# Kernel optimization log

Measured on AMD Instinct MI355X. Metric: run time of the kernel, lower is better.

## Reference

```python
import jax, jax.numpy as jnp
import numpy as np

N = 100000      # nodes
E = 3200000     # edges (avg degree 32)
NFEAT = 512
NHID = 256
NCLASS = 40
NLAYERS = 8
T1 = 5
T2 = 5
G1 = 1
G2 = 1
BETA = 0.5      # weight_beta
LAMDA = 0.5
ALPHA = 0.1
EPS = 1e-5


def ortho_trans(weight, T, groups):
    """Newton-Schulz orthogonalization (Ortho_Trans.forward)."""
    g = groups
    Z = weight.reshape(g, weight.shape[0] // g, -1)          # [g, d, k]
    Zc = Z - Z.mean(axis=-1, keepdims=True)
    S = jnp.einsum('gik,gjk->gij', Zc, Zc)                   # covariance [g, d, d]
    eye = jnp.eye(S.shape[-1], dtype=S.dtype)
    S = S + EPS * eye
    norm_S = jnp.sqrt(jnp.sum(S * S, axis=(1, 2), keepdims=True))  # fro norm
    S = S / norm_S
    B0 = jnp.broadcast_to(eye, S.shape)

    def body(B, _):
        B3 = B @ B @ B                                       # matrix_power3
        return 1.5 * B - 0.5 * (B3 @ S), None                # baddbmm(1.5,B,-0.5,B3,S)

    Bt, _ = jax.lax.scan(body, B0, None, length=T)
    W = (Bt @ Zc) / jnp.sqrt(norm_S)
    return W.reshape(weight.shape)


def setup_inputs() -> dict:
    key = jax.random.key(0)
    ks = jax.random.split(key, 8)
    stdv = 1.0 / np.sqrt(NHID)
    return {
        'x': jax.random.normal(ks[0], (N, NFEAT), dtype=jnp.float32),
        'edge_src': jax.random.randint(ks[1], (E,), 0, N, dtype=jnp.int32),
        'edge_dst': jax.random.randint(ks[2], (E,), 0, N, dtype=jnp.int32),
        'edge_weight': jax.random.uniform(ks[3], (E,), dtype=jnp.float32),
        'W0': jax.random.normal(ks[4], (NHID, NFEAT), dtype=jnp.float32) * 0.05,
        'b0': jnp.zeros((NHID,), dtype=jnp.float32),
        'convW': jax.random.uniform(ks[5], (NLAYERS, NHID, NHID), dtype=jnp.float32,
                                    minval=-stdv, maxval=stdv),
        'W1': jax.random.normal(ks[6], (NCLASS, NHID), dtype=jnp.float32) * 0.05,
        'b1': jnp.zeros((NCLASS,), dtype=jnp.float32),
    }


def reference(x, edge_src, edge_dst, edge_weight, W0, b0, convW, W1, b1):
    # fcs[0].weight is orthogonalized at init (Ortho=True)
    W0o = ortho_trans(W0, T1, G1)
    h = jax.nn.relu(x @ W0o.T + b0)                          # [N, NHID]
    h0 = h
    I = jnp.eye(NHID, dtype=h.dtype)
    ls = jnp.arange(1, NLAYERS + 1, dtype=h.dtype)

    def layer(h, inp):
        W, l = inp
        theta = jnp.log(LAMDA / l + 1.0)
        # sparse spmm: hi = adj @ h
        msgs = edge_weight[:, None] * h[edge_src]            # [E, NHID]
        hi = jax.ops.segment_sum(msgs, edge_dst, num_segments=N)
        support = (1.0 - ALPHA) * hi + ALPHA * h0            # variant=False -> r == support
        we = BETA * W + (1.0 - BETA) * I
        t = ortho_trans(we, T2, G2)
        out = jax.nn.relu(theta * (support @ t) + (1.0 - theta) * support)
        return out, None

    h, _ = jax.lax.scan(layer, h, (convW, ls))
    logits = h @ W1.T + b1
    return jax.nn.log_softmax(logits, axis=1)
```

## Files before the change

kernel.cpp:

```cpp
#include <hip/hip_runtime.h>
#include <math.h>

#define NNODES 100000
#define NEDGE  3200000
#define NF     512
#define NH     256
#define NC     40
#define NLAY   8
#define EPSV   1e-5f

#define NBUK 782
#define EPB  16384
#define BCAP 6144

typedef __attribute__((ext_vector_type(8))) short short8;
typedef __attribute__((ext_vector_type(4))) float floatx4;



__device__ __forceinline__ float block_sum_256(float v) {
    __shared__ float sb[8];
    #pragma unroll
    for (int off = 32; off; off >>= 1) v += __shfl_down(v, off, 64);
    if ((threadIdx.x & 63) == 0) sb[threadIdx.x >> 6] = v;
    __syncthreads();
    return sb[0] + sb[1] + sb[2] + sb[3];
}

__device__ __forceinline__ unsigned short bf16_rte(float a) {
    unsigned int u = __float_as_uint(a);
    return (unsigned short)((u + 0x7fffu + ((u >> 16) & 1u)) >> 16);
}
__device__ __forceinline__ unsigned int pack_bf2(float a, float b) {
    unsigned int ua = __float_as_uint(a), ub = __float_as_uint(b);
    ua = (ua + 0x7fffu + ((ua >> 16) & 1u)) >> 16;
    ub = (ub + 0x7fffu + ((ub >> 16) & 1u)) & 0xffff0000u;
    return ua | ub;
}


__global__ void k_hist(const int* __restrict__ dst, int* __restrict__ counts, int n) {
    int i = blockIdx.x * 256 + threadIdx.x;
    if (i < n) atomicAdd(&counts[dst[i]], 1);
}

__global__ void k_scan1(const int* __restrict__ in, int* __restrict__ out,
                        int* __restrict__ bsum, int n) {
    __shared__ int s[1024];
    int t = threadIdx.x, g = blockIdx.x * 1024 + t;
    int v = (g < n) ? in[g] : 0;
    s[t] = v; __syncthreads();
    for (int off = 1; off < 1024; off <<= 1) {
        int u = (t >= off) ? s[t - off] : 0;
        __syncthreads();
        s[t] += u;
        __syncthreads();
    }
    if (g < n) out[g] = s[t] - v;
    if (t == 1023) bsum[blockIdx.x] = s[1023];
}

__global__ void k_scan2(int* __restrict__ bsum, int nb) {
    __shared__ int s[128];
    int t = threadIdx.x;
    int v = (t < nb) ? bsum[t] : 0;
    s[t] = v; __syncthreads();
    for (int off = 1; off < 128; off <<= 1) {
        int u = (t >= off) ? s[t - off] : 0;
        __syncthreads();
        s[t] += u;
        __syncthreads();
    }
    if (t < nb) bsum[t] = s[t] - v;
}

__global__ void k_scan3(int* __restrict__ out, const int* __restrict__ bsum, int n) {
    int g = blockIdx.x * 1024 + threadIdx.x;
    if (g < n) out[g] += bsum[blockIdx.x];
}

__global__ void k_initcur(const int* __restrict__ rstart, int* __restrict__ gcur) {
    int b = blockIdx.x * 256 + threadIdx.x;
    if (b < NBUK) gcur[b] = rstart[b << 7];
}

__global__ __launch_bounds__(1024) void k_binA(const int* __restrict__ src,
                                               const int* __restrict__ dst,
                                               const float* __restrict__ w,
                                               int* __restrict__ gcur,
                                               uint2* __restrict__ gstage) {
    __shared__ int lhist[1024];
    __shared__ int lrun[NBUK];
    __shared__ int lcnt[NBUK];
    const int t = threadIdx.x;
    lhist[t] = 0;
    if (t < NBUK) lcnt[t] = 0;
    __syncthreads();
    const int e0 = blockIdx.x * EPB;
    unsigned int pk[16]; int bk[16]; int dl[16];
    #pragma unroll
    for (int i = 0; i < 16; i++) {
        int e = e0 + i * 1024 + t;
        bk[i] = -1;
        if (e < NEDGE) {
            int d = dst[e];
            bk[i] = d >> 7; dl[i] = d & 127;
            unsigned int wb = bf16_rte(w[e]) & 0x7FFFu;
            pk[i] = ((unsigned int)src[e] << 15) | wb;
            atomicAdd(&lhist[bk[i]], 1);
        }
    }
    __syncthreads();
    if (t < NBUK) {
        int c = lhist[t];
        if (c > 0) lrun[t] = atomicAdd(&gcur[t], c);
    }
    __syncthreads();
    #pragma unroll
    for (int i = 0; i < 16; i++) {
        if (bk[i] >= 0) {
            int p = lrun[bk[i]] + atomicAdd(&lcnt[bk[i]], 1);
            gstage[p] = make_uint2(pk[i], (unsigned int)dl[i]);
        }
    }
}

__global__ __launch_bounds__(256) void k_binB(const int* __restrict__ rstart,
                                              const uint2* __restrict__ gstage,
                                              unsigned int* __restrict__ epack) {
    __shared__ unsigned int  spk[BCAP];
    __shared__ unsigned char sdl[BCAP];
    __shared__ unsigned int  lout[BCAP];
    __shared__ int lh[256];
    const int b = blockIdx.x, t = threadIdx.x;
    const int base = rstart[b << 7];
    const int nn = (b + 1) << 7;
    const int end = (nn < NNODES) ? rstart[nn] : NEDGE;
    const int cnt = end - base;
    lh[t] = 0;
    __syncthreads();
    for (int i = t; i < cnt; i += 256) {
        uint2 e = gstage[base + i];
        spk[i] = e.x;
        int d = (int)(e.y & 127u);
        sdl[i] = (unsigned char)d;
        atomicAdd(&lh[d], 1);
    }
    __syncthreads();
    int v = lh[t];
    for (int off = 1; off < 256; off <<= 1) {
        int u = (t >= off) ? lh[t - off] : 0;
        __syncthreads();
        lh[t] += u;
        __syncthreads();
    }
    int excl = lh[t] - v;
    __syncthreads();
    lh[t] = excl;
    __syncthreads();
    for (int i = t; i < cnt; i += 256) {
        int p = atomicAdd(&lh[sdl[i]], 1);
        lout[p] = spk[i];
    }
    __syncthreads();
    for (int i = t; i < cnt; i += 256) epack[base + i] = lout[i];
}


__global__ void k_xbf16(const float* __restrict__ X, unsigned short* __restrict__ Xb, long n8) {
    long i = (long)blockIdx.x * 256 + threadIdx.x;
    if (i >= n8) return;
    const float* p = X + i * 8;
    float4 a = *(const float4*)p;
    float4 b = *(const float4*)(p + 4);
    uint4 o;
    o.x = pack_bf2(a.x, a.y); o.y = pack_bf2(a.z, a.w);
    o.z = pack_bf2(b.x, b.y); o.w = pack_bf2(b.z, b.w);
    *(uint4*)(Xb + i * 8) = o;
}


__global__ void k_zc0(const float* __restrict__ W0, float* __restrict__ Zc0) {
    int r = blockIdx.x, t = threadIdx.x;
    float a = W0[r * NF + t];
    float b = W0[r * NF + 256 + t];
    float mean = block_sum_256(a + b) * (1.0f / 512.0f);
    Zc0[r * NF + t]       = a - mean;
    Zc0[r * NF + 256 + t] = b - mean;
}

__global__ void k_zcC(const float* __restrict__ convW, float* __restrict__ ZcC) {
    int g = blockIdx.x >> 8, r = blockIdx.x & 255, t = threadIdx.x;
    float v = 0.5f * convW[((size_t)g * NH + r) * NH + t] + ((r == t) ? 0.5f : 0.0f);
    float mean = block_sum_256(v) * (1.0f / 256.0f);
    ZcC[((size_t)g * NH + r) * NH + t] = v - mean;
}

__global__ __launch_bounds__(256) void k_gram(const float* __restrict__ Zc0,
                                              const float* __restrict__ ZcC,
                                              float* __restrict__ S) {
    const int b = blockIdx.z;
    const float* A = (b == 0) ? Zc0 : (ZcC + (size_t)(b - 1) * 65536);
    const int K = (b == 0) ? 512 : 256;
    const int r0 = blockIdx.y * 64, c0 = blockIdx.x * 64;
    __shared__ float As[32][76], Bs[32][76];
    const int t = threadIdx.x, tx = t & 15, ty = t >> 4;
    const int lr = t >> 2, lk = (t & 3) * 4;
    float acc[4][4] = {};
    for (int k0 = 0; k0 < K; k0 += 32) {
        float4 a0 = *(const float4*)(A + (size_t)(r0 + lr) * K + k0 + lk);
        float4 a1 = *(const float4*)(A + (size_t)(r0 + lr) * K + k0 + lk + 16);
        As[lk + 0][lr] = a0.x; As[lk + 1][lr] = a0.y; As[lk + 2][lr] = a0.z; As[lk + 3][lr] = a0.w;
        As[lk + 16][lr] = a1.x; As[lk + 17][lr] = a1.y; As[lk + 18][lr] = a1.z; As[lk + 19][lr] = a1.w;
        float4 b0 = *(const float4*)(A + (size_t)(c0 + lr) * K + k0 + lk);
        float4 b1 = *(const float4*)(A + (size_t)(c0 + lr) * K + k0 + lk + 16);
        Bs[lk + 0][lr] = b0.x; Bs[lk + 1][lr] = b0.y; Bs[lk + 2][lr] = b0.z; Bs[lk + 3][lr] = b0.w;
        Bs[lk + 16][lr] = b1.x; Bs[lk + 17][lr] = b1.y; Bs[lk + 18][lr] = b1.z; Bs[lk + 19][lr] = b1.w;
        __syncthreads();
        #pragma unroll
        for (int kk = 0; kk < 32; kk++) {
            float a[4], bb[4];
            *(float4*)&a[0]  = *(const float4*)&As[kk][ty * 4];
            *(float4*)&bb[0] = *(const float4*)&Bs[kk][tx * 4];
            #pragma unroll
            for (int i = 0; i < 4; i++)
                #pragma unroll
                for (int j = 0; j < 4; j++) acc[i][j] = fmaf(a[i], bb[j], acc[i][j]);
        }
        __syncthreads();
    }
    #pragma unroll
    for (int i = 0; i < 4; i++)
        #pragma unroll
        for (int j = 0; j < 4; j++) {
            int r = r0 + ty * 4 + i, c = c0 + tx * 4 + j;
            float v = acc[i][j];
            if (r == c) v += EPSV;
            S[(size_t)b * 65536 + r * NH + c] = v;
        }
}

__global__ void k_fro(const float* __restrict__ S, float* __restrict__ scales) {
    __shared__ float sb[8];
    const int b = blockIdx.x, t = threadIdx.x;
    const float* p = S + (size_t)b * 65536;
    float s = 0.f;
    for (int i = t; i < 65536; i += 256) { float v = p[i]; s = fmaf(v, v, s); }
    #pragma unroll
    for (int off = 32; off; off >>= 1) s += __shfl_down(s, off, 64);
    if ((t & 63) == 0) sb[t >> 6] = s;
    __syncthreads();
    if (t == 0) {
        float nrm = sqrtf(sb[0] + sb[1] + sb[2] + sb[3]);
        scales[b]      = 1.0f / nrm;
        scales[16 + b] = rsqrtf(nrm);
    }
}

__global__ void k_initB1(const float* __restrict__ S, const float* __restrict__ scales,
                         float* __restrict__ B) {
    int i = blockIdx.x * 256 + threadIdx.x;
    int b = i >> 16, m = i & 65535;
    float v = -0.5f * scales[b] * S[i];
    if ((m >> 8) == (m & 255)) v += 1.5f;
    B[i] = v;
}

__global__ __launch_bounds__(256) void k_ns_pair(const float* __restrict__ Bb,
                                                 const float* __restrict__ Smat,
                                                 float* __restrict__ T1b,
                                                 float* __restrict__ T2b) {
    const int b = blockIdx.z;
    const int bb = (b < 9) ? b : b - 9;
    const float* A  = Bb + (size_t)bb * 65536;
    const float* Bm = (b < 9) ? A : (Smat + (size_t)bb * 65536);
    float* C = (b < 9) ? (T1b + (size_t)bb * 65536) : (T2b + (size_t)bb * 65536);
    const int r0 = blockIdx.y * 64, c0 = blockIdx.x * 64;
    __shared__ float As[32][76], Bs[32][76];
    const int t = threadIdx.x, tx = t & 15, ty = t >> 4;
    const int lr = t >> 2, lk = (t & 3) * 4;
    const int bk = t >> 3, bc = (t & 7) * 8;
    float acc[4][4] = {};
    for (int k0 = 0; k0 < 256; k0 += 32) {
        float4 a0 = *(const float4*)(A + (size_t)(r0 + lr) * 256 + k0 + lk);
        float4 a1 = *(const float4*)(A + (size_t)(r0 + lr) * 256 + k0 + lk + 16);
        As[lk + 0][lr] = a0.x; As[lk + 1][lr] = a0.y; As[lk + 2][lr] = a0.z; As[lk + 3][lr] = a0.w;
        As[lk + 16][lr] = a1.x; As[lk + 17][lr] = a1.y; As[lk + 18][lr] = a1.z; As[lk + 19][lr] = a1.w;
        float4 b0 = *(const float4*)(Bm + (size_t)(k0 + bk) * 256 + c0 + bc);
        float4 b1 = *(const float4*)(Bm + (size_t)(k0 + bk) * 256 + c0 + bc + 4);
        *(float4*)&Bs[bk][bc]     = b0;
        *(float4*)&Bs[bk][bc + 4] = b1;
        __syncthreads();
        #pragma unroll
        for (int kk = 0; kk < 32; kk++) {
            float a[4], bb2[4];
            *(float4*)&a[0]   = *(const float4*)&As[kk][ty * 4];
            *(float4*)&bb2[0] = *(const float4*)&Bs[kk][tx * 4];
            #pragma unroll
            for (int i = 0; i < 4; i++)
                #pragma unroll
                for (int j = 0; j < 4; j++) acc[i][j] = fmaf(a[i], bb2[j], acc[i][j]);
        }
        __syncthreads();
    }
    #pragma unroll
    for (int i = 0; i < 4; i++)
        #pragma unroll
        for (int j = 0; j < 4; j++)
            C[(size_t)(r0 + ty * 4 + i) * 256 + c0 + tx * 4 + j] = acc[i][j];
}

__global__ __launch_bounds__(256) void k_small_nn(const float* __restrict__ A0,
                                                  const float* __restrict__ B0,
                                                  float* __restrict__ C0,
                                                  int sA, int sB, int sC,
                                                  int K, int Ncols, int mode,
                                                  const float* __restrict__ scale) {
    const int b = blockIdx.z;
    const float* A = A0 + (size_t)b * sA;
    const float* Bm = B0 + (size_t)b * sB;
    float* C = C0 + (size_t)b * sC;
    const int r0 = blockIdx.y * 64, c0 = blockIdx.x * 64;
    __shared__ float As[32][76], Bs[32][76];
    const int t = threadIdx.x, tx = t & 15, ty = t >> 4;
    const int lr = t >> 2, lk = (t & 3) * 4;
    const int bk = t >> 3, bc = (t & 7) * 8;
    float acc[4][4] = {};
    for (int k0 = 0; k0 < K; k0 += 32) {
        float4 a0 = *(const float4*)(A + (size_t)(r0 + lr) * K + k0 + lk);
        float4 a1 = *(const float4*)(A + (size_t)(r0 + lr) * K + k0 + lk + 16);
        As[lk + 0][lr] = a0.x; As[lk + 1][lr] = a0.y; As[lk + 2][lr] = a0.z; As[lk + 3][lr] = a0.w;
        As[lk + 16][lr] = a1.x; As[lk + 17][lr] = a1.y; As[lk + 18][lr] = a1.z; As[lk + 19][lr] = a1.w;
        float4 b0 = *(const float4*)(Bm + (size_t)(k0 + bk) * Ncols + c0 + bc);
        float4 b1 = *(const float4*)(Bm + (size_t)(k0 + bk) * Ncols + c0 + bc + 4);
        *(float4*)&Bs[bk][bc]     = b0;
        *(float4*)&Bs[bk][bc + 4] = b1;
        __syncthreads();
        #pragma unroll
        for (int kk = 0; kk < 32; kk++) {
            float a[4], bb[4];
            *(float4*)&a[0]  = *(const float4*)&As[kk][ty * 4];
            *(float4*)&bb[0] = *(const float4*)&Bs[kk][tx * 4];
            #pragma unroll
            for (int i = 0; i < 4; i++)
                #pragma unroll
                for (int j = 0; j < 4; j++) acc[i][j] = fmaf(a[i], bb[j], acc[i][j]);
        }
        __syncthreads();
    }
    #pragma unroll
    for (int i = 0; i < 4; i++)
        #pragma unroll
        for (int j = 0; j < 4; j++) {
            size_t idx = (size_t)(r0 + ty * 4 + i) * Ncols + c0 + tx * 4 + j;
            if (mode == 1) C[idx] = 1.5f * C[idx] - 0.5f * scale[b] * acc[i][j];
            else C[idx] = scale[b] * acc[i][j];
        }
}


__global__ void k_prepM(const float* __restrict__ tbuf, unsigned short* __restrict__ Mpack) {
    int idx = blockIdx.x * 256 + threadIdx.x;
    int lane = idx & 63;
    int tg   = (idx >> 6) & 15;
    int s    = (idx >> 10) & 1;
    int c    = (idx >> 11) & 3;
    int l    = idx >> 13;
    float theta = logf(0.5f / (float)(l + 1) + 1.0f);
    float mtheta = 1.0f - theta;
    int n  = tg * 16 + (lane & 15);
    int k0 = c * 64 + s * 32 + (lane >> 4) * 8;
    const float* T = tbuf + (size_t)l * 65536;
    unsigned short o[8];
    #pragma unroll
    for (int j = 0; j < 8; j++) {
        int kp = k0 + j;
        int kn = (kp & 0xC0) | ((kp & 3) << 4) | ((kp >> 2) & 15);
        float v = theta * T[(size_t)kn * 256 + n] + ((kn == n) ? mtheta : 0.0f);
        o[j] = bf16_rte(v);
    }
    *(uint4*)(Mpack + (size_t)idx * 8) = *(uint4*)o;
}

__global__ void k_prepW0(const float* __restrict__ W0o, unsigned short* __restrict__ Wpack) {
    int idx = blockIdx.x * 256 + threadIdx.x;
    int lane = idx & 63;
    int tg   = (idx >> 6) & 15;
    int s    = (idx >> 10) & 1;
    int c    = idx >> 11;
    int n  = tg * 16 + (lane & 15);
    int k0 = c * 64 + s * 32 + (lane >> 4) * 8;
    const float* p = W0o + (size_t)n * NF + k0;
    unsigned short o[8];
    #pragma unroll
    for (int j = 0; j < 8; j++) o[j] = bf16_rte(p[j]);
    *(uint4*)(Wpack + (size_t)idx * 8) = *(uint4*)o;
}


__global__ __launch_bounds__(256) void k_fc0_mfma(const unsigned short* __restrict__ Xb,
                                                  const unsigned short* __restrict__ Wp,
                                                  const float* __restrict__ bias,
                                                  unsigned char* __restrict__ h0u8,
                                                  float* __restrict__ h0scale) {
    __shared__ int rmax[64];
    const int t = threadIdx.x, lane = t & 63, w = t >> 6;
    const int q = lane >> 4, m = lane & 15;
    const int r0 = blockIdx.x * 64;
    if (t < 64) rmax[t] = 0;
    floatx4 acc[4][4] = {};
    #pragma unroll
    for (int c = 0; c < 8; c++) {
        #pragma unroll
        for (int s = 0; s < 2; s++) {
            short8 afr[4];
            #pragma unroll
            for (int i = 0; i < 4; i++) {
                int row = r0 + i * 16 + m; if (row > NNODES - 1) row = NNODES - 1;
                afr[i] = *(const short8*)(Xb + (size_t)row * NF + c * 64 + s * 32 + q * 8);
            }
            #pragma unroll
            for (int tg = 0; tg < 4; tg++) {
                short8 bfr = *(const short8*)(Wp + (size_t)c * 16384 + s * 8192
                                              + (w * 4 + tg) * 512 + lane * 8);
                #pragma unroll
                for (int i = 0; i < 4; i++)
                    acc[i][tg] = __builtin_amdgcn_mfma_f32_16x16x32_bf16(afr[i], bfr, acc[i][tg], 0, 0, 0);
            }
        }
    }
    #pragma unroll
    for (int tg = 0; tg < 4; tg++) {
        float bv = bias[w * 64 + tg * 16 + m];
        #pragma unroll
        for (int i = 0; i < 4; i++)
            #pragma unroll
            for (int r = 0; r < 4; r++)
                acc[i][tg][r] = fmaxf(acc[i][tg][r] + bv, 0.f);
    }
    __syncthreads();
    #pragma unroll
    for (int i = 0; i < 4; i++)
        #pragma unroll
        for (int r = 0; r < 4; r++) {
            float mx = fmaxf(fmaxf(acc[i][0][r], acc[i][1][r]),
                             fmaxf(acc[i][2][r], acc[i][3][r]));
            mx = fmaxf(mx, __shfl_xor(mx, 1));
            mx = fmaxf(mx, __shfl_xor(mx, 2));
            mx = fmaxf(mx, __shfl_xor(mx, 4));
            mx = fmaxf(mx, __shfl_xor(mx, 8));
            if (m == 0) atomicMax(&rmax[i * 16 + q * 4 + r], __float_as_int(mx));
        }
    __syncthreads();
    #pragma unroll
    for (int i = 0; i < 4; i++)
        #pragma unroll
        for (int r = 0; r < 4; r++) {
            int row = r0 + i * 16 + q * 4 + r;
            if (row >= NNODES) continue;
            float rm = __int_as_float(rmax[i * 16 + q * 4 + r]);
            float qs = rm > 0.f ? 255.0f / rm : 0.f;
            unsigned int b0 = (unsigned int)fmaf(acc[i][0][r], qs, 0.5f);
            unsigned int b1 = (unsigned int)fmaf(acc[i][1][r], qs, 0.5f);
            unsigned int b2 = (unsigned int)fmaf(acc[i][2][r], qs, 0.5f);
            unsigned int b3 = (unsigned int)fmaf(acc[i][3][r], qs, 0.5f);
            *(unsigned int*)(h0u8 + (size_t)row * NH + w * 64 + m * 4) =
                b0 | (b1 << 8) | (b2 << 16) | (b3 << 24);
        }
    if (t < 64 && r0 + t < NNODES)
        h0scale[r0 + t] = __int_as_float(rmax[t]) * (1.0f / 255.0f);
}


__global__ __launch_bounds__(256) void k_spmm(const int* __restrict__ rstart,
                                              const int* __restrict__ counts,
                                              const unsigned int* __restrict__ epack,
                                              const unsigned char* __restrict__ hu8,
                                              const float* __restrict__ hscale,
                                              const unsigned char* __restrict__ h0u8,
                                              const float* __restrict__ h0scale,
                                              unsigned short* __restrict__ supbf) {
    __shared__ int2 se[4][64];
    const int wv = threadIdx.x >> 6, lane = threadIdx.x & 63;
    const int node = blockIdx.x * 4 + wv;
    const int start = rstart[node], deg = counts[node];
    float a0 = 0.f, a1 = 0.f, a2 = 0.f, a3 = 0.f;
    for (int base = 0; base < deg; base += 64) {
        int j = base + lane;
        if (j < deg) {
            unsigned int u = epack[start + j];
            int s = (int)(u >> 15);
            float wt = __uint_as_float((u & 0x7FFFu) << 16);
            se[wv][lane] = make_int2(s, __float_as_int(wt * hscale[s] * 0.9f));
        }
        int mm = deg - base; if (mm > 64) mm = 64;
        int e = 0;
        for (; e + 8 <= mm; e += 8) {
            float ww[8]; unsigned int g[8];
            #pragma unroll
            for (int u = 0; u < 8; u++) {
                int2 ed = se[wv][e + u];
                ww[u] = __int_as_float(ed.y);
                g[u] = *(const unsigned int*)(hu8 + ((size_t)ed.x << 8) + (lane << 2));
            }
            #pragma unroll
            for (int u = 0; u < 8; u++) {
                a0 = fmaf(ww[u], (float)(g[u] & 0xFFu), a0);
                a1 = fmaf(ww[u], (float)((g[u] >> 8) & 0xFFu), a1);
                a2 = fmaf(ww[u], (float)((g[u] >> 16) & 0xFFu), a2);
                a3 = fmaf(ww[u], (float)(g[u] >> 24), a3);
            }
        }
        for (; e < mm; e++) {
            int2 ed = se[wv][e];
            float ww = __int_as_float(ed.y);
            unsigned int g = *(const unsigned int*)(hu8 + ((size_t)ed.x << 8) + (lane << 2));
            a0 = fmaf(ww, (float)(g & 0xFFu), a0);
            a1 = fmaf(ww, (float)((g >> 8) & 0xFFu), a1);
            a2 = fmaf(ww, (float)((g >> 16) & 0xFFu), a2);
            a3 = fmaf(ww, (float)(g >> 24), a3);
        }
    }
    unsigned int rg = *(const unsigned int*)(h0u8 + ((size_t)node << 8) + (lane << 2));
    float rs = h0scale[node] * 0.1f;
    float o0 = fmaf(rs, (float)(rg & 0xFFu), a0);
    float o1 = fmaf(rs, (float)((rg >> 8) & 0xFFu), a1);
    float o2 = fmaf(rs, (float)((rg >> 16) & 0xFFu), a2);
    float o3 = fmaf(rs, (float)(rg >> 24), a3);
    uint2 ov;
    ov.x = pack_bf2(o0, o1);
    ov.y = pack_bf2(o2, o3);
    *(uint2*)(supbf + ((size_t)node << 8) + (lane << 2)) = ov;
}


__global__ __launch_bounds__(256) void k_gemm_layer(const unsigned short* __restrict__ Sbf,
                                                    const unsigned short* __restrict__ Mp,
                                                    unsigned char* __restrict__ out_u8,
                                                    float* __restrict__ out_scale,
                                                    unsigned short* __restrict__ out_bf) {
    __shared__ int rmax[64];
    const int t = threadIdx.x, lane = t & 63, w = t >> 6;
    const int q = lane >> 4, m = lane & 15;
    const int r0 = blockIdx.x * 64;
    if (t < 64) rmax[t] = 0;
    floatx4 acc[4][4] = {};
    #pragma unroll
    for (int c = 0; c < 4; c++) {
        #pragma unroll
        for (int s = 0; s < 2; s++) {
            short8 afr[4];
            #pragma unroll
            for (int i = 0; i < 4; i++) {
                int row = r0 + i * 16 + m; if (row > NNODES - 1) row = NNODES - 1;
                afr[i] = *(const short8*)(Sbf + (size_t)row * NH + c * 64 + s * 32 + q * 8);
            }
            #pragma unroll
            for (int tg = 0; tg < 4; tg++) {
                short8 bfr = *(const short8*)(Mp + (size_t)c * 16384 + s * 8192
                                              + (w * 4 + tg) * 512 + lane * 8);
                #pragma unroll
                for (int i = 0; i < 4; i++)
                    acc[i][tg] = __builtin_amdgcn_mfma_f32_16x16x32_bf16(afr[i], bfr, acc[i][tg], 0, 0, 0);
            }
        }
    }
    #pragma unroll
    for (int i = 0; i < 4; i++)
        #pragma unroll
        for (int tg = 0; tg < 4; tg++)
            #pragma unroll
            for (int r = 0; r < 4; r++)
                acc[i][tg][r] = fmaxf(acc[i][tg][r], 0.f);

    if (out_bf) {
        #pragma unroll
        for (int i = 0; i < 4; i++)
            #pragma unroll
            for (int tg = 0; tg < 4; tg++) {
                int col = w * 64 + tg * 16 + m;
                #pragma unroll
                for (int r = 0; r < 4; r++) {
                    int row = r0 + i * 16 + q * 4 + r;
                    if (row >= NNODES) continue;
                    out_bf[(size_t)row * NH + col] = bf16_rte(acc[i][tg][r]);
                }
            }
        return;
    }
    __syncthreads();
    #pragma unroll
    for (int i = 0; i < 4; i++)
        #pragma unroll
        for (int r = 0; r < 4; r++) {
            float mx = fmaxf(fmaxf(acc[i][0][r], acc[i][1][r]),
                             fmaxf(acc[i][2][r], acc[i][3][r]));
            mx = fmaxf(mx, __shfl_xor(mx, 1));
            mx = fmaxf(mx, __shfl_xor(mx, 2));
            mx = fmaxf(mx, __shfl_xor(mx, 4));
            mx = fmaxf(mx, __shfl_xor(mx, 8));
            if (m == 0) atomicMax(&rmax[i * 16 + q * 4 + r], __float_as_int(mx));
        }
    __syncthreads();
    #pragma unroll
    for (int i = 0; i < 4; i++)
        #pragma unroll
        for (int r = 0; r < 4; r++) {
            int row = r0 + i * 16 + q * 4 + r;
            if (row >= NNODES) continue;
            float rm = __int_as_float(rmax[i * 16 + q * 4 + r]);
            float qs = rm > 0.f ? 255.0f / rm : 0.f;
            unsigned int b0 = (unsigned int)fmaf(acc[i][0][r], qs, 0.5f);
            unsigned int b1 = (unsigned int)fmaf(acc[i][1][r], qs, 0.5f);
            unsigned int b2 = (unsigned int)fmaf(acc[i][2][r], qs, 0.5f);
            unsigned int b3 = (unsigned int)fmaf(acc[i][3][r], qs, 0.5f);
            *(unsigned int*)(out_u8 + (size_t)row * NH + w * 64 + m * 4) =
                b0 | (b1 << 8) | (b2 << 16) | (b3 << 24);
        }
    if (t < 64 && r0 + t < NNODES)
        out_scale[r0 + t] = __int_as_float(rmax[t]) * (1.0f / 255.0f);
}


__global__ __launch_bounds__(256) void k_logits(const unsigned short* __restrict__ hb,
                                                const float* __restrict__ W1,
                                                const float* __restrict__ b1,
                                                float* __restrict__ out, int nrows) {
    __shared__ float hs[32][260];
    __shared__ float Ws[40][260];
    __shared__ float ls[32][44];
    __shared__ float lse[32];
    const int t = threadIdx.x;
    const int row0 = blockIdx.x * 32;
    for (int i = t; i < 40 * 64; i += 256) {
        int c = i >> 6, k4 = i & 63;
        *(float4*)&Ws[c][k4 * 4] = *(const float4*)(W1 + (size_t)c * NH + k4 * 4);
    }
    for (int i = t; i < 32 * 32; i += 256) {
        int r = i >> 5, k8 = i & 31;
        int gr = row0 + r;
        uint4 v = make_uint4(0u, 0u, 0u, 0u);
        if (gr < nrows) v = *(const uint4*)(hb + ((size_t)gr << 8) + k8 * 8);
        float* d = &hs[r][k8 * 8];
        d[0] = __uint_as_float(v.x << 16); d[1] = __uint_as_float(v.x & 0xffff0000u);
        d[2] = __uint_as_float(v.y << 16); d[3] = __uint_as_float(v.y & 0xffff0000u);
        d[4] = __uint_as_float(v.z << 16); d[5] = __uint_as_float(v.z & 0xffff0000u);
        d[6] = __uint_as_float(v.w << 16); d[7] = __uint_as_float(v.w & 0xffff0000u);
    }
    __syncthreads();
    const int r = t & 31, cg = t >> 5;
    float acc[5];
    #pragma unroll
    for (int j = 0; j < 5; j++) acc[j] = b1[cg * 5 + j];
    for (int k = 0; k < NH; k++) {
        float hv = hs[r][k];
        #pragma unroll
        for (int j = 0; j < 5; j++) acc[j] = fmaf(hv, Ws[cg * 5 + j][k], acc[j]);
    }
    #pragma unroll
    for (int j = 0; j < 5; j++) ls[r][cg * 5 + j] = acc[j];
    __syncthreads();
    if (t < 32) {
        float m = -3.4e38f;
        for (int c = 0; c < NC; c++) m = fmaxf(m, ls[t][c]);
        float s = 0.f;
        for (int c = 0; c < NC; c++) s += expf(ls[t][c] - m);
        lse[t] = m + logf(s);
    }
    __syncthreads();
    for (int i = t; i < 32 * NC; i += 256) {
        int r2 = i / NC, c = i % NC;
        int gr = row0 + r2;
        if (gr < nrows) out[(size_t)gr * NC + c] = ls[r2][c] - lse[r2];
    }
}


extern "C" void kernel_launch(void* const* d_in, const int* in_sizes, int n_in,
                              void* d_out, int out_size, void* d_ws, size_t ws_size,
                              hipStream_t stream) {
    const float* x      = (const float*)d_in[0];
    const int*   e_src  = (const int*)d_in[1];
    const int*   e_dst  = (const int*)d_in[2];
    const float* e_w    = (const float*)d_in[3];
    const float* W0     = (const float*)d_in[4];
    const float* b0     = (const float*)d_in[5];
    const float* convW  = (const float*)d_in[6];
    const float* W1     = (const float*)d_in[7];
    const float* b1     = (const float*)d_in[8];
    float* out = (float*)d_out;

    char* ws = (char*)d_ws;
    const size_t OFF_H0U8   = 0;
    const size_t OFF_HU8A   = OFF_H0U8 + (size_t)NNODES * NH;
    const size_t OFF_HU8B   = OFF_HU8A + (size_t)NNODES * NH;
    const size_t OFF_H0SC   = OFF_HU8B + (size_t)NNODES * NH;
    const size_t OFF_SCA    = OFF_H0SC + (size_t)NNODES * 4;
    const size_t OFF_SCB    = OFF_SCA + (size_t)NNODES * 4;
    const size_t OFF_SUPBF  = OFF_SCB + (size_t)NNODES * 4;
    const size_t OFF_HBF    = OFF_SUPBF + (size_t)NNODES * NH * 2;
    const size_t OFF_XBF    = OFF_HBF + (size_t)NNODES * NH * 2;
    const size_t OFF_EPACK  = OFF_XBF + (size_t)NNODES * NF * 2;
    const size_t OFF_RSTART = OFF_EPACK + (size_t)NEDGE * 4;
    const size_t OFF_COUNTS = OFF_RSTART + (size_t)NNODES * 4;
    const size_t OFF_CURSOR = OFF_COUNTS + (size_t)NNODES * 4;
    const size_t OFF_BSUM   = OFF_CURSOR + (size_t)NNODES * 4;
    const size_t OFF_ZC0    = OFF_BSUM + 1024;
    const size_t OFF_ZCC    = OFF_ZC0 + 256 * 512 * 4;
    const size_t OFF_S      = OFF_ZCC + 8 * 65536 * 4;
    const size_t OFF_B      = OFF_S + 9 * 65536 * 4;
    const size_t OFF_T1     = OFF_B + 9 * 65536 * 4;
    const size_t OFF_T2     = OFF_T1 + 9 * 65536 * 4;
    const size_t OFF_T      = OFF_T2 + 9 * 65536 * 4;
    const size_t OFF_W0O    = OFF_T + 8 * 65536 * 4;
    const size_t OFF_SCALES = OFF_W0O + 256 * 512 * 4;
    const size_t OFF_MPACK  = OFF_SCALES + 1024;
    const size_t OFF_WPACK  = OFF_MPACK + 8 * 65536 * 2;

    unsigned char* h0u8 = (unsigned char*)(ws + OFF_H0U8);
    unsigned char* hu8A = (unsigned char*)(ws + OFF_HU8A);
    unsigned char* hu8B = (unsigned char*)(ws + OFF_HU8B);
    float* h0sc = (float*)(ws + OFF_H0SC);
    float* scA  = (float*)(ws + OFF_SCA);
    float* scB  = (float*)(ws + OFF_SCB);
    unsigned short* supbf = (unsigned short*)(ws + OFF_SUPBF);
    unsigned short* hbf   = (unsigned short*)(ws + OFF_HBF);
    unsigned short* xbf   = (unsigned short*)(ws + OFF_XBF);
    unsigned int* epack  = (unsigned int*)(ws + OFF_EPACK);
    int*    rstart = (int*)(ws + OFF_RSTART);
    int*    counts = (int*)(ws + OFF_COUNTS);
    int*    gcur   = (int*)(ws + OFF_CURSOR);
    int*    bsum   = (int*)(ws + OFF_BSUM);
    float*  Zc0    = (float*)(ws + OFF_ZC0);
    float*  ZcC    = (float*)(ws + OFF_ZCC);
    float*  Smat   = (float*)(ws + OFF_S);
    float*  Bb     = (float*)(ws + OFF_B);
    float*  T1b    = (float*)(ws + OFF_T1);
    float*  T2b    = (float*)(ws + OFF_T2);
    float*  tbuf   = (float*)(ws + OFF_T);
    float*  W0o    = (float*)(ws + OFF_W0O);
    float*  scales = (float*)(ws + OFF_SCALES);
    unsigned short* Mpack = (unsigned short*)(ws + OFF_MPACK);
    unsigned short* Wpack = (unsigned short*)(ws + OFF_WPACK);
    uint2* gstage = (uint2*)(ws + OFF_SUPBF);

    (void)in_sizes; (void)n_in; (void)out_size; (void)ws_size;

    hipMemsetAsync(counts, 0, (size_t)NNODES * 4, stream);
    k_hist<<<(NEDGE + 255) / 256, 256, 0, stream>>>(e_dst, counts, NEDGE);
    const int NB = (NNODES + 1023) / 1024;
    k_scan1<<<NB, 1024, 0, stream>>>(counts, rstart, bsum, NNODES);
    k_scan2<<<1, 128, 0, stream>>>(bsum, NB);
    k_scan3<<<NB, 1024, 0, stream>>>(rstart, bsum, NNODES);
    k_initcur<<<4, 256, 0, stream>>>(rstart, gcur);
    k_binA<<<(NEDGE + EPB - 1) / EPB, 1024, 0, stream>>>(e_src, e_dst, e_w, gcur, gstage);
    k_binB<<<NBUK, 256, 0, stream>>>(rstart, gstage, epack);

    const long N8 = (long)NNODES * NF / 8;
    k_xbf16<<<(int)((N8 + 255) / 256), 256, 0, stream>>>(x, xbf, N8);

    k_zc0<<<256, 256, 0, stream>>>(W0, Zc0);
    k_zcC<<<8 * 256, 256, 0, stream>>>(convW, ZcC);
    k_gram<<<dim3(4, 4, 9), 256, 0, stream>>>(Zc0, ZcC, Smat);
    k_fro<<<9, 256, 0, stream>>>(Smat, scales);
    k_initB1<<<9 * 256, 256, 0, stream>>>(Smat, scales, Bb);
    for (int it = 1; it < 5; it++) {
        k_ns_pair<<<dim3(4, 4, 18), 256, 0, stream>>>(Bb, Smat, T1b, T2b);
        k_small_nn<<<dim3(4, 4, 9), 256, 0, stream>>>(T1b, T2b, Bb, 65536, 65536, 65536,
                                                      256, 256, 1, scales);
    }
    k_small_nn<<<dim3(8, 4, 1), 256, 0, stream>>>(Bb, Zc0, W0o, 0, 0, 0,
                                                  256, 512, 2, scales + 16);
    k_small_nn<<<dim3(4, 4, 8), 256, 0, stream>>>(Bb + 65536, ZcC, tbuf, 65536, 65536, 65536,
                                                  256, 256, 2, scales + 17);

    k_prepM<<<256, 256, 0, stream>>>(tbuf, Mpack);
    k_prepW0<<<64, 256, 0, stream>>>(W0o, Wpack);

    const int GB = (NNODES + 63) / 64;
    k_fc0_mfma<<<GB, 256, 0, stream>>>(xbf, Wpack, b0, h0u8, h0sc);

    const unsigned char* hin = h0u8;
    const float* hinsc = h0sc;
    unsigned char* u8bufs[2] = { hu8A, hu8B };
    float* scbufs[2] = { scA, scB };
    for (int l = 1; l <= NLAY; l++) {
        k_spmm<<<NNODES / 4, 256, 0, stream>>>(rstart, counts, epack, hin, hinsc,
                                               h0u8, h0sc, supbf);
        const unsigned short* Mp = Mpack + (size_t)(l - 1) * 65536;
        if (l == NLAY) {
            k_gemm_layer<<<GB, 256, 0, stream>>>(supbf, Mp, nullptr, nullptr, hbf);
        } else {
            unsigned char* ou = u8bufs[(l - 1) & 1];
            float* os = scbufs[(l - 1) & 1];
            k_gemm_layer<<<GB, 256, 0, stream>>>(supbf, Mp, ou, os, nullptr);
            hin = ou; hinsc = os;
        }
    }

    k_logits<<<(NNODES + 31) / 32, 256, 0, stream>>>(hbf, W1, b1, out, NNODES);
}
```

Baseline: 2.321 ms.

## Build CSR via bucket histogram and derive per-node offsets inside binning

```diff
diff --git a/kernel.cpp b/kernel.cpp
--- a/kernel.cpp
+++ b/kernel.cpp
@@ -39,16 +39,31 @@
 }
 
 
-__global__ void k_hist(const int* __restrict__ dst, int* __restrict__ counts, int n) {
-    int i = blockIdx.x * 256 + threadIdx.x;
-    if (i < n) atomicAdd(&counts[dst[i]], 1);
-}
-
-__global__ void k_scan1(const int* __restrict__ in, int* __restrict__ out,
-                        int* __restrict__ bsum, int n) {
+__global__ __launch_bounds__(1024) void k_histbuk(const int* __restrict__ dst,
+                                                  int* __restrict__ bcnt) {
+    __shared__ int lh[NBUK];
+    const int t = threadIdx.x;
+    if (t < NBUK) lh[t] = 0;
+    __syncthreads();
+    const int e0 = blockIdx.x * EPB;
+    #pragma unroll
+    for (int i = 0; i < 16; i++) {
+        int e = e0 + i * 1024 + t;
+        if (e < NEDGE) atomicAdd(&lh[dst[e] >> 7], 1);
+    }
+    __syncthreads();
+    if (t < NBUK) {
+        int c = lh[t];
+        if (c) atomicAdd(&bcnt[t], c);
+    }
+}
+
+__global__ __launch_bounds__(1024) void k_scanbuk(const int* __restrict__ bcnt,
+                                                  int* __restrict__ bstart,
+                                                  int* __restrict__ gcur) {
     __shared__ int s[1024];
-    int t = threadIdx.x, g = blockIdx.x * 1024 + t;
-    int v = (g < n) ? in[g] : 0;
+    const int t = threadIdx.x;
+    int v = (t < NBUK) ? bcnt[t] : 0;
     s[t] = v; __syncthreads();
     for (int off = 1; off < 1024; off <<= 1) {
         int u = (t >= off) ? s[t - off] : 0;
@@ -56,32 +71,12 @@
         s[t] += u;
         __syncthreads();
     }
-    if (g < n) out[g] = s[t] - v;
-    if (t == 1023) bsum[blockIdx.x] = s[1023];
-}
-
-__global__ void k_scan2(int* __restrict__ bsum, int nb) {
-    __shared__ int s[128];
-    int t = threadIdx.x;
-    int v = (t < nb) ? bsum[t] : 0;
-    s[t] = v; __syncthreads();
-    for (int off = 1; off < 128; off <<= 1) {
-        int u = (t >= off) ? s[t - off] : 0;
-        __syncthreads();
-        s[t] += u;
-        __syncthreads();
-    }
-    if (t < nb) bsum[t] = s[t] - v;
-}
-
-__global__ void k_scan3(int* __restrict__ out, const int* __restrict__ bsum, int n) {
-    int g = blockIdx.x * 1024 + threadIdx.x;
-    if (g < n) out[g] += bsum[blockIdx.x];
-}
-
-__global__ void k_initcur(const int* __restrict__ rstart, int* __restrict__ gcur) {
-    int b = blockIdx.x * 256 + threadIdx.x;
-    if (b < NBUK) gcur[b] = rstart[b << 7];
+    if (t < NBUK) {
+        int e = s[t] - v;
+        bstart[t] = e;
+        gcur[t] = e;
+    }
+    if (t == NBUK - 1) bstart[NBUK] = s[t];
 }
 
 __global__ __launch_bounds__(1024) void k_binA(const int* __restrict__ src,
@@ -125,17 +120,18 @@
     }
 }
 
-__global__ __launch_bounds__(256) void k_binB(const int* __restrict__ rstart,
+__global__ __launch_bounds__(256) void k_binB(const int* __restrict__ bstart,
                                               const uint2* __restrict__ gstage,
-                                              unsigned int* __restrict__ epack) {
+                                              unsigned int* __restrict__ epack,
+                                              int* __restrict__ rstart,
+                                              int* __restrict__ counts) {
     __shared__ unsigned int  spk[BCAP];
     __shared__ unsigned char sdl[BCAP];
     __shared__ unsigned int  lout[BCAP];
     __shared__ int lh[256];
     const int b = blockIdx.x, t = threadIdx.x;
-    const int base = rstart[b << 7];
-    const int nn = (b + 1) << 7;
-    const int end = (nn < NNODES) ? rstart[nn] : NEDGE;
+    const int base = bstart[b];
+    const int end  = bstart[b + 1];
     const int cnt = end - base;
     lh[t] = 0;
     __syncthreads();
@@ -157,6 +153,10 @@
     int excl = lh[t] - v;
     __syncthreads();
     lh[t] = excl;
+    if (t < 128) {
+        int node = (b << 7) + t;
+        if (node < NNODES) { rstart[node] = base + excl; counts[node] = v; }
+    }
     __syncthreads();
     for (int i = t; i < cnt; i += 256) {
         int p = atomicAdd(&lh[sdl[i]], 1);
@@ -730,7 +730,8 @@
     int*    rstart = (int*)(ws + OFF_RSTART);
     int*    counts = (int*)(ws + OFF_COUNTS);
     int*    gcur   = (int*)(ws + OFF_CURSOR);
-    int*    bsum   = (int*)(ws + OFF_BSUM);
+    int*    bcnt   = (int*)(ws + OFF_CURSOR + 4096);
+    int*    bstart = (int*)(ws + OFF_CURSOR + 8192);
     float*  Zc0    = (float*)(ws + OFF_ZC0);
     float*  ZcC    = (float*)(ws + OFF_ZCC);
     float*  Smat   = (float*)(ws + OFF_S);
@@ -746,15 +747,12 @@
 
     (void)in_sizes; (void)n_in; (void)out_size; (void)ws_size;
 
-    hipMemsetAsync(counts, 0, (size_t)NNODES * 4, stream);
-    k_hist<<<(NEDGE + 255) / 256, 256, 0, stream>>>(e_dst, counts, NEDGE);
-    const int NB = (NNODES + 1023) / 1024;
-    k_scan1<<<NB, 1024, 0, stream>>>(counts, rstart, bsum, NNODES);
-    k_scan2<<<1, 128, 0, stream>>>(bsum, NB);
-    k_scan3<<<NB, 1024, 0, stream>>>(rstart, bsum, NNODES);
-    k_initcur<<<4, 256, 0, stream>>>(rstart, gcur);
-    k_binA<<<(NEDGE + EPB - 1) / EPB, 1024, 0, stream>>>(e_src, e_dst, e_w, gcur, gstage);
-    k_binB<<<NBUK, 256, 0, stream>>>(rstart, gstage, epack);
+    hipMemsetAsync(bcnt, 0, (size_t)NBUK * 4, stream);
+    const int NBA = (NEDGE + EPB - 1) / EPB;
+    k_histbuk<<<NBA, 1024, 0, stream>>>(e_dst, bcnt);
+    k_scanbuk<<<1, 1024, 0, stream>>>(bcnt, bstart, gcur);
+    k_binA<<<NBA, 1024, 0, stream>>>(e_src, e_dst, e_w, gcur, gstage);
+    k_binB<<<NBUK, 256, 0, stream>>>(bstart, gstage, epack, rstart, counts);
 
     const long N8 = (long)NNODES * NF / 8;
     k_xbf16<<<(int)((N8 + 255) / 256), 256, 0, stream>>>(x, xbf, N8);
```

Result: faster. 2.215 ms (-4.6%).
